# Kernel optimization log

Hardware: AMD Instinct MI355X
Metric: run time of the kernel (lower is better)

## Reference

```python
import jax, jax.numpy as jnp
import numpy as np

D_MODEL = 1024
NUM_HEADS = 16
HEAD_DIM = D_MODEL // NUM_HEADS


def setup_inputs() -> dict:
    key = jax.random.key(0)
    ks = jax.random.split(key, 9)
    s = 1.0 / np.sqrt(D_MODEL)
    inp = {"x": jax.random.normal(ks[0], (2, 2048, D_MODEL), dtype=jnp.float32)}
    for i, name in enumerate(["q", "k", "v", "o"]):
        inp[f"W_{name}"] = jax.random.uniform(ks[1 + i], (D_MODEL, D_MODEL), dtype=jnp.float32, minval=-s, maxval=s)
        inp[f"b_{name}"] = jax.random.uniform(ks[5 + i], (D_MODEL,), dtype=jnp.float32, minval=-s, maxval=s)
    return inp


def reference(x, W_q, b_q, W_k, b_k, W_v, b_v, W_o, b_o):
    B, S, _ = x.shape
    def split_heads(t):  # [B,S,D] -> [B,H,S,Dh]
        return t.reshape(B, S, NUM_HEADS, HEAD_DIM).transpose(0, 2, 1, 3)
    q = split_heads(x @ W_q.T + b_q)
    k = split_heads(x @ W_k.T + b_k)
    v = split_heads(x @ W_v.T + b_v)
    scale = 1.0 / np.sqrt(HEAD_DIM).astype(np.float32)
    scores = jnp.einsum('bhqd,bhkd->bhqk', q, k) * scale  # [B,H,S,S]
    attn = jax.nn.softmax(scores, axis=-1)
    out = jnp.einsum('bhqk,bhkd->bhqd', attn, v)  # [B,H,S,Dh]
    out = out.transpose(0, 2, 1, 3).reshape(B, S, D_MODEL)
    return out @ W_o.T + b_o
```

## Files before the change

kernel.cpp:

```cpp
#include <hip/hip_runtime.h>
#include <hip/hip_bf16.h>

typedef __attribute__((ext_vector_type(8))) short short8;
typedef __attribute__((ext_vector_type(4))) float f32x4;
typedef __attribute__((ext_vector_type(16))) float f32x16;
typedef unsigned short ushort_t;
typedef unsigned int uint_t;

#define LOG2E 1.4426950408889634f

#if __has_builtin(__builtin_amdgcn_exp2f)
#define EXP2(x) __builtin_amdgcn_exp2f(x)
#else
#define EXP2(x) exp2f(x)
#endif

__device__ __forceinline__ ushort_t f2bf(float f) {
    union { float f; unsigned int i; } x; x.f = f;
    unsigned int r = x.i + 0x7FFF + ((x.i >> 16) & 1);
    return (ushort_t)(r >> 16);
}
__device__ __forceinline__ float bf2f(ushort_t u) {
    union { unsigned int i; float f; } x; x.i = ((unsigned int)u) << 16; return x.f;
}
__device__ __forceinline__ uint_t cvtpk(float lo, float hi) {
    uint_t r;
    asm("v_cvt_pk_bf16_f32 %0, %1, %2" : "=v"(r) : "v"(lo), "v"(hi));
    return r;
}

__device__ __forceinline__ void gll16(const void* g, void* l) {
    __builtin_amdgcn_global_load_lds((const __attribute__((address_space(1))) unsigned int*)g,
                                     (__attribute__((address_space(3))) unsigned int*)l,
                                     16, 0, 0);
}

__device__ __forceinline__ int xcd_lin() {
    int gx = gridDim.x;
    int n  = gx * gridDim.y;
    int lin = blockIdx.y * gx + blockIdx.x;
    int cpx = n >> 3;
    return (lin & 7) * cpx + (lin >> 3);
}

__global__ __launch_bounds__(256) void convert_kernel(
    const float* __restrict__ x,
    const float* __restrict__ Wq, const float* __restrict__ Wk,
    const float* __restrict__ Wv, const float* __restrict__ Wo,
    const float* __restrict__ bq, const float* __restrict__ bk, const float* __restrict__ bv,
    ushort_t* __restrict__ xb, ushort_t* __restrict__ wqkv,
    ushort_t* __restrict__ wob, float* __restrict__ bqkv)
{
    int idx = blockIdx.x * 256 + threadIdx.x;
    const float* src; ushort_t* dst; int off;
    if (idx < 1048576) { src = x; dst = xb; off = idx * 4; }
    else if (idx < 1835008) {
        int e = (idx - 1048576) * 4;
        int wi = e >> 20; off = e & 1048575;
        src = (wi == 0) ? Wq : ((wi == 1) ? Wk : Wv);
        dst = wqkv + ((size_t)wi << 20);
    } else { off = (idx - 1835008) * 4; src = Wo; dst = wob; }
    float4 v = *reinterpret_cast<const float4*>(src + off);
    ushort_t o0 = f2bf(v.x), o1 = f2bf(v.y), o2 = f2bf(v.z), o3 = f2bf(v.w);
    ushort_t* d = dst + off;
    d[0] = o0; d[1] = o1; d[2] = o2; d[3] = o3;
    if (idx < 768) {
        int wi = idx >> 8; int o4 = (idx & 255) * 4;
        const float* bsrc = (wi == 0) ? bq : ((wi == 1) ? bk : bv);
        *reinterpret_cast<float4*>(bqkv + wi * 1024 + o4) =
            *reinterpret_cast<const float4*>(bsrc + o4);
    }
}

template<int WRITE_BF16, int BN>
__global__ __launch_bounds__(256) void gemm_nt(
    const ushort_t* __restrict__ A, const ushort_t* __restrict__ Bm,
    const float* __restrict__ bias, void* __restrict__ Cout,
    int M, int N, int K)
{
    constexpr int NT = BN / 32;
    __shared__ ushort_t As[2][128 * 32];
    __shared__ ushort_t Bs[2][BN * 32];

    const int tid  = threadIdx.x;
    const int lane = tid & 63;
    const int wv   = tid >> 6;

    const int sw = xcd_lin();
    const int bx = sw % gridDim.x;
    const int by = sw / gridDim.x;
    const int m0 = by * 128;
    const int n0 = bx * BN;

    const int wr   = wv >> 1, wc = wv & 1;
    const int g    = lane >> 4, c = lane & 15;

    f32x4 acc[4][NT] = {};

    const int srow = lane >> 2;
    const int scol = (lane & 3) * 8;
    const ushort_t* Ag = A  + (size_t)(m0 + wv * 32 + srow) * K + scol;
    const ushort_t* Bg = Bm + (size_t)(n0 + (BN == 128 ? wv * 32 : wv * 16) + srow) * K + scol;

    auto STAGE = [&](int b, int k0) {
        gll16(Ag + k0,          &As[b][(wv * 32) * 32]);
        gll16(Ag + 16 * K + k0, &As[b][(wv * 32 + 16) * 32]);
        if (BN == 128) {
            gll16(Bg + k0,          &Bs[b][(wv * 32) * 32]);
            gll16(Bg + 16 * K + k0, &Bs[b][(wv * 32 + 16) * 32]);
        } else {
            gll16(Bg + k0,          &Bs[b][(wv * 16) * 32]);
        }
    };

    STAGE(0, 0);
    int cur = 0;
    for (int k0 = 0; k0 < K; k0 += 32) {
        if (k0 + 32 < K) {
            STAGE(cur ^ 1, k0 + 32);
            if (BN == 128) asm volatile("s_waitcnt vmcnt(4)" ::: "memory");
            else           asm volatile("s_waitcnt vmcnt(3)" ::: "memory");
        } else {
            asm volatile("s_waitcnt vmcnt(0)" ::: "memory");
        }
        __builtin_amdgcn_sched_barrier(0);
        __builtin_amdgcn_s_barrier();
        __builtin_amdgcn_sched_barrier(0);

        short8 af[4], bf[NT];
        #pragma unroll
        for (int i = 0; i < 4; i++)
            af[i] = *reinterpret_cast<const short8*>(&As[cur][(wr * 64 + i * 16 + c) * 32 + g * 8]);
        #pragma unroll
        for (int j = 0; j < NT; j++)
            bf[j] = *reinterpret_cast<const short8*>(&Bs[cur][(wc * (BN / 2) + j * 16 + c) * 32 + g * 8]);
        #pragma unroll
        for (int i = 0; i < 4; i++)
            #pragma unroll
            for (int j = 0; j < NT; j++)
                acc[i][j] = __builtin_amdgcn_mfma_f32_16x16x32_bf16(af[i], bf[j], acc[i][j], 0, 0, 0);

        asm volatile("s_waitcnt lgkmcnt(0)" ::: "memory");
        __builtin_amdgcn_sched_barrier(0);
        __builtin_amdgcn_s_barrier();
        __builtin_amdgcn_sched_barrier(0);
        cur ^= 1;
    }

    #pragma unroll
    for (int i = 0; i < 4; i++) {
        int row = m0 + wr * 64 + i * 16 + 4 * g;
        #pragma unroll
        for (int j = 0; j < NT; j++) {
            int col = n0 + wc * (BN / 2) + j * 16 + c;
            float bv_ = bias[col];
            #pragma unroll
            for (int r = 0; r < 4; r++) {
                float v = acc[i][j][r] + bv_;
                if (WRITE_BF16)
                    ((ushort_t*)Cout)[(size_t)(row + r) * N + col] = f2bf(v);
                else
                    ((float*)Cout)[(size_t)(row + r) * N + col] = v;
            }
        }
    }
}

__global__ __launch_bounds__(256) void vtrans_kernel(
    const ushort_t* __restrict__ qkv, ushort_t* __restrict__ Vt)
{
    __shared__ ushort_t T[256 * 64];
    const int tid = threadIdx.x;
    const int st0 = blockIdx.x * 256;
    const int bh  = blockIdx.y;
    const int b = bh >> 4, h = bh & 15;
    const ushort_t* vg = qkv + (size_t)b * 2048 * 3072 + 2048 + h * 64;

    #pragma unroll
    for (int p = 0; p < 8; p++) {
        int tok = p * 32 + (tid >> 3);
        int ch  = (tid & 7) ^ (tok & 7);
        short8 v = *reinterpret_cast<const short8*>(
            vg + (size_t)(st0 + tok) * 3072 + (tid & 7) * 8);
        *reinterpret_cast<short8*>(&T[tok * 64 + ch * 8]) = v;
    }
    __syncthreads();
    const int d = tid >> 2;
    ushort_t* og = Vt + ((size_t)bh * 64 + d) * 2048 + st0;
    #pragma unroll
    for (int it = 0; it < 8; it++) {
        int sc_ = (tid & 3) + 4 * it;
        short8 v;
        #pragma unroll
        for (int e = 0; e < 8; e++) {
            int s = sc_ * 8 + e;
            v[e] = (short)T[s * 64 + (((d >> 3) ^ (s & 7)) * 8) + (d & 7)];
        }
        *reinterpret_cast<short8*>(og + sc_ * 8) = v;
    }
}

__global__ __launch_bounds__(512, 4) void attn_kernel(
    const ushort_t* __restrict__ qkv, const ushort_t* __restrict__ Vt,
    ushort_t* __restrict__ out)
{
    __shared__ ushort_t smem[32768];

    const int tid  = threadIdx.x;
    const int lane = tid & 63;
    const int wv   = tid >> 6;
    const int wvi  = wv & 3;
    const int g2   = wv >> 2;
    const int sw   = xcd_lin();
    const int qt   = sw & 15;
    const int bh   = sw >> 4;
    const int b = bh >> 4, h = bh & 15;
    const int c  = lane & 31;
    const int hh = lane >> 5;

    const int q0 = qt * 128 + wvi * 32;
    const size_t tokbase = (size_t)b * 2048;

    short8 qf[4];
    {
        const ushort_t* qg = qkv + (tokbase + q0 + c) * 3072 + h * 64 + hh * 8;
        #pragma unroll
        for (int s = 0; s < 4; s++) {
            short8 v = *reinterpret_cast<const short8*>(qg + s * 16);
            short8 o;
            #pragma unroll
            for (int e = 0; e < 8; e++)
                o[e] = (short)f2bf(bf2f((ushort_t)v[e]) * (0.125f * LOG2E));
            qf[s] = o;
        }
    }

    const int l8 = lane & 7;
    const int l3 = lane >> 3;
    const ushort_t* kg0 = qkv + (tokbase + g2 * 1024 + wvi * 16 + l3) * 3072
                              + 1024 + h * 64 + (l8 ^ l3) * 8;
    const ushort_t* vg0 = Vt + ((size_t)bh * 64 + wvi * 16 + l3) * 2048
                             + g2 * 1024 + (l8 ^ l3) * 8;

    f32x16 oacc[2] = {};
    f32x16 sc[2];
    float l0 = 0.f, l1 = 0.f, l2 = 0.f, l3s = 0.f;

    auto STAGE = [&](int bb, int kt) {
        char* Kd = (char*)smem + g2 * 32768 + bb * 16384 + wvi * 2048;
        char* Vd = Kd + 8192;
        const ushort_t* ks = kg0 + (size_t)(kt * 64) * 3072;
        gll16(ks,                     Kd);
        gll16(ks + (size_t)8 * 3072,  Kd + 1024);
        const ushort_t* vs = vg0 + kt * 64;
        gll16(vs,            Vd);
        gll16(vs + 8 * 2048, Vd + 1024);
    };

    STAGE(0, 0);
    __syncthreads();
    int cur = 0;

    for (int it = 0; it < 16; it++) {
        if (it + 1 < 16) STAGE(cur ^ 1, it + 1);

        const char* KlB = (const char*)smem + g2 * 32768 + cur * 16384;
        const char* VlB = KlB + 8192;

        sc[0] = f32x16{}; sc[1] = f32x16{};
        __builtin_amdgcn_s_setprio(1);
        #pragma unroll
        for (int st = 0; st < 4; st++) {
            const int chB = (((2 * st + hh) ^ (c & 7)) << 4);
            short8 ak0 = *reinterpret_cast<const short8*>(KlB + (c     ) * 128 + chB);
            short8 ak1 = *reinterpret_cast<const short8*>(KlB + (32 + c) * 128 + chB);
            sc[0] = __builtin_amdgcn_mfma_f32_32x32x16_bf16(ak0, qf[st], sc[0], 0, 0, 0);
            sc[1] = __builtin_amdgcn_mfma_f32_32x32x16_bf16(ak1, qf[st], sc[1], 0, 0, 0);
        }
        __builtin_amdgcn_s_setprio(0);

        #pragma unroll
        for (int t = 0; t < 2; t++) {
            #pragma unroll
            for (int r = 0; r < 16; r += 4) {
                sc[t][r]   = EXP2(sc[t][r]);   l0  += sc[t][r];
                sc[t][r+1] = EXP2(sc[t][r+1]); l1  += sc[t][r+1];
                sc[t][r+2] = EXP2(sc[t][r+2]); l2  += sc[t][r+2];
                sc[t][r+3] = EXP2(sc[t][r+3]); l3s += sc[t][r+3];
            }
        }

        __builtin_amdgcn_s_setprio(1);
        #pragma unroll
        for (int s = 0; s < 4; s++) {
            const int t0 = s >> 1;
            const int rb = (s & 1) * 8;
            uint_t A0 = cvtpk(sc[t0][rb + 0], sc[t0][rb + 1]);
            uint_t B0 = cvtpk(sc[t0][rb + 2], sc[t0][rb + 3]);
            uint_t A1 = cvtpk(sc[t0][rb + 4], sc[t0][rb + 5]);
            uint_t B1 = cvtpk(sc[t0][rb + 6], sc[t0][rb + 7]);
            uint_t sendA = hh ? A0 : A1;
            uint_t sendB = hh ? B0 : B1;
            uint_t recvA = (uint_t)__shfl_xor((int)sendA, 32);
            uint_t recvB = (uint_t)__shfl_xor((int)sendB, 32);
            uint_t d0 = hh ? recvA : A0;
            uint_t d1 = hh ? recvB : B0;
            uint_t d2 = hh ? A1 : recvA;
            uint_t d3 = hh ? B1 : recvB;
            union { uint_t u[4]; short8 s8; } pu;
            pu.u[0] = d0; pu.u[1] = d1; pu.u[2] = d2; pu.u[3] = d3;

            const int chB = (((2 * s + hh) ^ (c & 7)) << 4);
            short8 av0 = *reinterpret_cast<const short8*>(VlB + (c     ) * 128 + chB);
            short8 av1 = *reinterpret_cast<const short8*>(VlB + (32 + c) * 128 + chB);
            oacc[0] = __builtin_amdgcn_mfma_f32_32x32x16_bf16(av0, pu.s8, oacc[0], 0, 0, 0);
            oacc[1] = __builtin_amdgcn_mfma_f32_32x32x16_bf16(av1, pu.s8, oacc[1], 0, 0, 0);
        }
        __builtin_amdgcn_s_setprio(0);

        __syncthreads();
        cur ^= 1;
    }

    float l_own = (l0 + l1) + (l2 + l3s);
    float* dump = (float*)smem;
    const int di = (wvi * 64 + lane) * 34;
    if (g2) {
        #pragma unroll
        for (int r = 0; r < 16; r++) { dump[di + r] = oacc[0][r]; dump[di + 16 + r] = oacc[1][r]; }
        dump[di + 32] = l_own;
    }
    __syncthreads();
    if (!g2) {
        #pragma unroll
        for (int r = 0; r < 16; r++) { oacc[0][r] += dump[di + r]; oacc[1][r] += dump[di + 16 + r]; }
        l_own += dump[di + 32];
        float l_tot = l_own + __shfl_xor(l_own, 32);
        float invl = 1.0f / l_tot;

        ushort_t* Olw = (ushort_t*)((char*)smem + 36864 + wvi * 4608);
        #pragma unroll
        for (int td = 0; td < 2; td++)
            #pragma unroll
            for (int rr = 0; rr < 4; rr++)
                #pragma unroll
                for (int j2 = 0; j2 < 2; j2++) {
                    int r = 4 * rr + 2 * j2;
                    float v0 = (td == 0) ? oacc[0][r] : oacc[1][r];
                    float v1 = (td == 0) ? oacc[0][r + 1] : oacc[1][r + 1];
                    uint_t wd = cvtpk(v0 * invl, v1 * invl);
                    int dcol = 32 * td + 4 * hh + 8 * rr + 2 * j2;
                    *reinterpret_cast<uint_t*>(&Olw[c * 72 + dcol]) = wd;
                }
        int row = lane >> 1;
        int e0  = (lane & 1) * 32;
        ushort_t* og = out + (tokbase + q0 + row) * 1024 + h * 64 + e0;
        #pragma unroll
        for (int k2 = 0; k2 < 4; k2++) {
            short8 v;
            #pragma unroll
            for (int e = 0; e < 8; e++) v[e] = (short)Olw[row * 72 + e0 + k2 * 8 + e];
            *reinterpret_cast<short8*>(og + k2 * 8) = v;
        }
    }
}

extern "C" void kernel_launch(void* const* d_in, const int* in_sizes, int n_in,
                              void* d_out, int out_size, void* d_ws, size_t ws_size,
                              hipStream_t stream) {
    const float* x  = (const float*)d_in[0];
    const float* Wq = (const float*)d_in[1];
    const float* bq = (const float*)d_in[2];
    const float* Wk = (const float*)d_in[3];
    const float* bk = (const float*)d_in[4];
    const float* Wv = (const float*)d_in[5];
    const float* bv = (const float*)d_in[6];
    const float* Wo = (const float*)d_in[7];
    const float* bo = (const float*)d_in[8];

    uintptr_t w = (uintptr_t)d_ws;
    ushort_t* xb    = (ushort_t*)w;  w += 8388608;
    ushort_t* wqkv  = (ushort_t*)w;  w += 6291456;
    ushort_t* wob   = (ushort_t*)w;  w += 2097152;
    float*    bqkv  = (float*)w;     w += 12288;
    ushort_t* qkv   = (ushort_t*)w;  w += 25165824;
    ushort_t* attno = (ushort_t*)w;  w += 8388608;
    ushort_t* Vt    = xb;

    convert_kernel<<<8192, 256, 0, stream>>>(x, Wq, Wk, Wv, Wo, bq, bk, bv,
                                             xb, wqkv, wob, bqkv);
    gemm_nt<1, 128><<<dim3(24, 32), 256, 0, stream>>>(xb, wqkv, bqkv, qkv, 4096, 3072, 1024);
    vtrans_kernel<<<dim3(8, 32), 256, 0, stream>>>(qkv, Vt);
    attn_kernel<<<dim3(16, 32), 512, 0, stream>>>(qkv, Vt, attno);
    gemm_nt<0, 64><<<dim3(16, 32), 256, 0, stream>>>(attno, wob, bo, (void*)d_out, 4096, 1024, 1024);
}
```

Before: 117.2 us.

## Fuse V transpose into QKV GEMM epilogue and refine attention pipeline barriers

```diff
diff --git a/kernel.cpp b/kernel.cpp
--- a/kernel.cpp
+++ b/kernel.cpp
@@ -72,10 +72,11 @@
     }
 }
 
-template<int WRITE_BF16, int BN>
+template<int WRITE_BF16, int BN, int WRITE_VT>
 __global__ __launch_bounds__(256) void gemm_nt(
     const ushort_t* __restrict__ A, const ushort_t* __restrict__ Bm,
     const float* __restrict__ bias, void* __restrict__ Cout,
+    ushort_t* __restrict__ Vt,
     int M, int N, int K)
 {
     constexpr int NT = BN / 32;
@@ -154,49 +155,33 @@
         for (int j = 0; j < NT; j++) {
             int col = n0 + wc * (BN / 2) + j * 16 + c;
             float bv_ = bias[col];
-            #pragma unroll
-            for (int r = 0; r < 4; r++) {
-                float v = acc[i][j][r] + bv_;
-                if (WRITE_BF16)
-                    ((ushort_t*)Cout)[(size_t)(row + r) * N + col] = f2bf(v);
-                else
-                    ((float*)Cout)[(size_t)(row + r) * N + col] = v;
+            float v0 = acc[i][j][0] + bv_;
+            float v1 = acc[i][j][1] + bv_;
+            float v2 = acc[i][j][2] + bv_;
+            float v3 = acc[i][j][3] + bv_;
+            if (WRITE_VT && col >= 2048) {
+                int dcol = col - 2048;
+                int hv = dcol >> 6, dd = dcol & 63;
+                int bb = row >> 11, ss = row & 2047;
+                uint_t w0 = cvtpk(v0, v1);
+                uint_t w1 = cvtpk(v2, v3);
+                uint_t* vp = reinterpret_cast<uint_t*>(
+                    Vt + (((size_t)(bb * 16 + hv) * 64 + dd) * 2048 + ss));
+                vp[0] = w0; vp[1] = w1;
+            } else if (WRITE_BF16) {
+                ushort_t* cp = (ushort_t*)Cout;
+                cp[(size_t)(row + 0) * N + col] = f2bf(v0);
+                cp[(size_t)(row + 1) * N + col] = f2bf(v1);
+                cp[(size_t)(row + 2) * N + col] = f2bf(v2);
+                cp[(size_t)(row + 3) * N + col] = f2bf(v3);
+            } else {
+                float* cp = (float*)Cout;
+                cp[(size_t)(row + 0) * N + col] = v0;
+                cp[(size_t)(row + 1) * N + col] = v1;
+                cp[(size_t)(row + 2) * N + col] = v2;
+                cp[(size_t)(row + 3) * N + col] = v3;
             }
         }
-    }
-}
-
-__global__ __launch_bounds__(256) void vtrans_kernel(
-    const ushort_t* __restrict__ qkv, ushort_t* __restrict__ Vt)
-{
-    __shared__ ushort_t T[256 * 64];
-    const int tid = threadIdx.x;
-    const int st0 = blockIdx.x * 256;
-    const int bh  = blockIdx.y;
-    const int b = bh >> 4, h = bh & 15;
-    const ushort_t* vg = qkv + (size_t)b * 2048 * 3072 + 2048 + h * 64;
-
-    #pragma unroll
-    for (int p = 0; p < 8; p++) {
-        int tok = p * 32 + (tid >> 3);
-        int ch  = (tid & 7) ^ (tok & 7);
-        short8 v = *reinterpret_cast<const short8*>(
-            vg + (size_t)(st0 + tok) * 3072 + (tid & 7) * 8);
-        *reinterpret_cast<short8*>(&T[tok * 64 + ch * 8]) = v;
-    }
-    __syncthreads();
-    const int d = tid >> 2;
-    ushort_t* og = Vt + ((size_t)bh * 64 + d) * 2048 + st0;
-    #pragma unroll
-    for (int it = 0; it < 8; it++) {
-        int sc_ = (tid & 3) + 4 * it;
-        short8 v;
-        #pragma unroll
-        for (int e = 0; e < 8; e++) {
-            int s = sc_ * 8 + e;
-            v[e] = (short)T[s * 64 + (((d >> 3) ^ (s & 7)) * 8) + (d & 7)];
-        }
-        *reinterpret_cast<short8*>(og + sc_ * 8) = v;
     }
 }
 
@@ -258,11 +243,18 @@
     };
 
     STAGE(0, 0);
-    __syncthreads();
     int cur = 0;
 
     for (int it = 0; it < 16; it++) {
-        if (it + 1 < 16) STAGE(cur ^ 1, it + 1);
+        if (it + 1 < 16) {
+            STAGE(cur ^ 1, it + 1);
+            asm volatile("s_waitcnt vmcnt(4)" ::: "memory");
+        } else {
+            asm volatile("s_waitcnt vmcnt(0)" ::: "memory");
+        }
+        __builtin_amdgcn_sched_barrier(0);
+        __builtin_amdgcn_s_barrier();
+        __builtin_amdgcn_sched_barrier(0);
 
         const char* KlB = (const char*)smem + g2 * 32768 + cur * 16384;
         const char* VlB = KlB + 8192;
@@ -318,7 +310,10 @@
         }
         __builtin_amdgcn_s_setprio(0);
 
-        __syncthreads();
+        asm volatile("s_waitcnt lgkmcnt(0)" ::: "memory");
+        __builtin_amdgcn_sched_barrier(0);
+        __builtin_amdgcn_s_barrier();
+        __builtin_amdgcn_sched_barrier(0);
         cur ^= 1;
     }
 
@@ -385,12 +380,11 @@
     float*    bqkv  = (float*)w;     w += 12288;
     ushort_t* qkv   = (ushort_t*)w;  w += 25165824;
     ushort_t* attno = (ushort_t*)w;  w += 8388608;
-    ushort_t* Vt    = xb;
+    ushort_t* Vt    = (ushort_t*)w;  w += 8388608;
 
     convert_kernel<<<8192, 256, 0, stream>>>(x, Wq, Wk, Wv, Wo, bq, bk, bv,
                                              xb, wqkv, wob, bqkv);
-    gemm_nt<1, 128><<<dim3(24, 32), 256, 0, stream>>>(xb, wqkv, bqkv, qkv, 4096, 3072, 1024);
-    vtrans_kernel<<<dim3(8, 32), 256, 0, stream>>>(qkv, Vt);
+    gemm_nt<1, 128, 1><<<dim3(24, 32), 256, 0, stream>>>(xb, wqkv, bqkv, qkv, Vt, 4096, 3072, 1024);
     attn_kernel<<<dim3(16, 32), 512, 0, stream>>>(qkv, Vt, attno);
-    gemm_nt<0, 64><<<dim3(16, 32), 256, 0, stream>>>(attno, wob, bo, (void*)d_out, 4096, 1024, 1024);
-}
+    gemm_nt<0, 64, 0><<<dim3(16, 32), 256, 0, stream>>>(attno, wob, bo, (void*)d_out, nullptr, 4096, 1024, 1024);
+}
```

After: 111.9 us. 1.05x faster.
